# Optimization experiments

Measured on AMD Instinct MI355X. Metric: run time of the kernel, lower is better.

## Reference

```python
import jax, jax.numpy as jnp
import numpy as np
from jax import lax

SR = 7
HEADS = 8
EPS = 1e-5

def dwconv(x, w):
    # x: [B,C,H,W], w: [C,1,3,3] depthwise
    return lax.conv_general_dilated(x, w, (1, 1), 'SAME',
                                    feature_group_count=x.shape[1],
                                    dimension_numbers=('NCHW', 'OIHW', 'NCHW'))

def bn(x, g, b, m, v):
    # eval-mode BatchNorm2d over channel dim of [B,C,H,W]
    scale = g / jnp.sqrt(v + EPS)
    return x * scale[:, None, None] + (b - m * scale)[:, None, None]

def avgpool(x, k):
    B, C, H, W = x.shape
    return x.reshape(B, C, H // k, k, W // k, k).mean(axis=(3, 5))

def upsample(x, k):
    B, C, H, W = x.shape
    return jax.image.resize(x, (B, C, H * k, W * k), method='bilinear')


def setup_inputs() -> dict:
    key = jax.random.key(0)
    ks = jax.random.split(key, 12)
    B, N, C = 16, 3136, 256
    d = {}
    d['x'] = jax.random.normal(ks[0], (B, N, C), jnp.float32)
    d['Wv'] = jax.random.normal(ks[1], (C, C), jnp.float32) * 0.05
    d['conv1_w'] = jax.random.normal(ks[2], (C, 1, 3, 3), jnp.float32) * 0.05
    d['bn1_g'] = jnp.ones((C,), jnp.float32)
    d['bn1_b'] = jnp.zeros((C,), jnp.float32)
    d['bn1_m'] = jax.random.normal(ks[3], (C,), jnp.float32) * 0.05
    d['bn1_v'] = jax.random.uniform(ks[4], (C,), jnp.float32, 0.5, 1.5)
    d['conv2_w'] = jax.random.normal(ks[5], (C, 1, 3, 3), jnp.float32) * 0.05
    d['bn2_g'] = jnp.ones((C,), jnp.float32)
    d['bn2_b'] = jnp.zeros((C,), jnp.float32)
    d['bn2_m'] = jax.random.normal(ks[6], (C,), jnp.float32) * 0.05
    d['bn2_v'] = jax.random.uniform(ks[7], (C,), jnp.float32, 0.5, 1.5)
    d['vup_w'] = jax.random.normal(ks[8], (C, 1, 3, 3), jnp.float32) * 0.05
    d['bn3_g'] = jnp.ones((C,), jnp.float32)
    d['bn3_b'] = jnp.zeros((C,), jnp.float32)
    d['bn3_m'] = jax.random.normal(ks[9], (C,), jnp.float32) * 0.05
    d['bn3_v'] = jax.random.uniform(ks[10], (C,), jnp.float32, 0.5, 1.5)
    d['Wp'] = jax.random.normal(ks[11], (C, C), jnp.float32) * 0.05
    d['bp'] = jnp.zeros((C,), jnp.float32)
    return d


def reference(x, Wv, conv1_w, bn1_g, bn1_b, bn1_m, bn1_v,
              conv2_w, bn2_g, bn2_b, bn2_m, bn2_v,
              vup_w, bn3_g, bn3_b, bn3_m, bn3_v, Wp, bp):
    B, N, C = x.shape
    h = w = int(np.sqrt(N))
    hd = C // HEADS
    scale = C ** (-0.5)

    v = x @ Wv.T                                    # [B,N,C] (torch Linear, no bias)
    skip = v.reshape(B, h, w, C).transpose(0, 3, 1, 2)  # [B,C,h,w]

    s1 = bn(dwconv(skip, conv1_w), bn1_g, bn1_b, bn1_m, bn1_v)
    q = avgpool(s1, SR)                             # [B,C,h_,w_]
    s2 = bn(dwconv(jax.nn.gelu(s1, approximate=False), conv2_w),
            bn2_g, bn2_b, bn2_m, bn2_v)
    k = avgpool(s2, SR)                             # [B,C,h_,w_]
    skip_tok = jax.nn.gelu(s2, approximate=False).reshape(B, C, N).transpose(0, 2, 1)

    h_, w_ = h // SR, w // SR
    N_ = h_ * w_
    qh = q.reshape(B, HEADS, hd, N_).transpose(0, 1, 3, 2)   # [B,H,N_,d]
    kh = k.reshape(B, HEADS, hd, N_).transpose(0, 1, 3, 2)   # [B,H,N_,d]
    vh = v.reshape(B, N, HEADS, hd).transpose(0, 2, 1, 3)    # [B,H,N,d]

    attn = jnp.einsum('bhnd,bhmd->bhnm', qh, kh)             # [B,H,N_,N_]
    attn = attn.reshape(B * HEADS, N_, h_, w_)
    attn = upsample(attn, SR) * scale                        # [B*H,N_,h,w]
    attn = attn.reshape(B, HEADS, N_, N)
    attn = jax.nn.softmax(attn, axis=-1)

    o = jnp.einsum('bhnm,bhmd->bhnd', attn, vh)              # [B,H,N_,d]
    o = o.reshape(B, HEADS, h_, w_, hd).transpose(0, 1, 4, 2, 3).reshape(B, C, h_, w_)
    o = bn(dwconv(upsample(o, SR), vup_w), bn3_g, bn3_b, bn3_m, bn3_v)  # [B,C,h,w]

    out = o.reshape(B, C, N).transpose(0, 2, 1) + skip_tok
    out = out @ Wp.T + bp
    return out
```

## Files before the change

### kernel.cpp

```cpp
#include <hip/hip_runtime.h>
#include <math.h>

#define B_     16
#define H_IMG  56
#define W_IMG  56
#define N_TOK  3136
#define C_     256
#define C4_    64
#define NHEAD  8
#define HDIM   32
#define NCH    8

typedef float f32x4 __attribute__((ext_vector_type(4)));
typedef __bf16 bf16x8 __attribute__((ext_vector_type(8)));

__device__ __forceinline__ float geluf(float x) {
    return 0.5f * x * (1.0f + erff(x * 0.70710678118654752f));
}

__device__ __forceinline__ void up_coef(int o, int& i0, int& i1, float& t) {
    float f  = (float)(o - 3) * (1.0f / 7.0f);
    float fl = floorf(f);
    int   ii = (int)fl;
    t = f - fl;
    if (ii < 0)       { i0 = 0; i1 = 0; t = 0.0f; }
    else if (ii >= 7) { i0 = 7; i1 = 7; t = 0.0f; }
    else              { i0 = ii; i1 = ii + 1; }
}

__device__ __forceinline__ void split_bf16(float4 f, uint2& hi, uint2& lo) {
    unsigned u0 = __float_as_uint(f.x), u1 = __float_as_uint(f.y);
    unsigned u2 = __float_as_uint(f.z), u3 = __float_as_uint(f.w);
    unsigned h0 = u0 & 0xFFFF0000u, h1 = u1 & 0xFFFF0000u;
    unsigned h2 = u2 & 0xFFFF0000u, h3 = u3 & 0xFFFF0000u;
    hi = make_uint2((h0 >> 16) | h1, (h2 >> 16) | h3);
    float l0 = f.x - __uint_as_float(h0);
    float l1 = f.y - __uint_as_float(h1);
    float l2 = f.z - __uint_as_float(h2);
    float l3 = f.w - __uint_as_float(h3);
    lo = make_uint2((__float_as_uint(l0) >> 16) | (__float_as_uint(l1) & 0xFFFF0000u),
                    (__float_as_uint(l2) >> 16) | (__float_as_uint(l3) & 0xFFFF0000u));
}

__device__ __forceinline__ unsigned pack2_bf16(float a, float b) {
    __bf16 ha = (__bf16)a, hb = (__bf16)b;
    unsigned short ua = __builtin_bit_cast(unsigned short, ha);
    unsigned short ub = __builtin_bit_cast(unsigned short, hb);
    return (unsigned)ua | ((unsigned)ub << 16);
}

__global__ void prep_kernel(
    const float* __restrict__ w1, const float* __restrict__ w2, const float* __restrict__ w3,
    const float* __restrict__ g1, const float* __restrict__ b1, const float* __restrict__ m1, const float* __restrict__ v1,
    const float* __restrict__ g2, const float* __restrict__ b2, const float* __restrict__ m2, const float* __restrict__ v2,
    const float* __restrict__ g3, const float* __restrict__ b3, const float* __restrict__ m3, const float* __restrict__ v3,
    float* __restrict__ wT1, float* __restrict__ wT2, float* __restrict__ wT3,
    float* __restrict__ sc1, float* __restrict__ sh1,
    float* __restrict__ sc2, float* __restrict__ sh2,
    float* __restrict__ sc3, float* __restrict__ sh3)
{
    int c = threadIdx.x;
#pragma unroll
    for (int t = 0; t < 9; ++t) {
        wT1[t * C_ + c] = w1[c * 9 + t];
        wT2[t * C_ + c] = w2[c * 9 + t];
        wT3[t * C_ + c] = w3[c * 9 + t];
    }
    float s1 = g1[c] * rsqrtf(v1[c] + 1e-5f); sc1[c] = s1; sh1[c] = b1[c] - m1[c] * s1;
    float s2 = g2[c] * rsqrtf(v2[c] + 1e-5f); sc2[c] = s2; sh2[c] = b2[c] - m2[c] * s2;
    float s3 = g3[c] * rsqrtf(v3[c] + 1e-5f); sc3[c] = s3; sh3[c] = b3[c] - m3[c] * s3;
}

#define AHI 0
#define ALO 2560
#define BHI 5120
#define BLO 7680
__global__ __launch_bounds__(256, 2) void gemm_nt_mfma_kernel(
    const float* __restrict__ A,
    const float* __restrict__ Bm,
    const float* __restrict__ bias,
    float* __restrict__ C,
    int M, int N)
{
    __shared__ unsigned lds[10240];
    const int tid  = threadIdx.x;
    const int nb   = N >> 7;
    const int bx   = blockIdx.x % nb;
    const int by   = blockIdx.x / nb;
    const int lane = tid & 63;
    const int wv   = tid >> 6;
    const int wr   = wv >> 1, wc = wv & 1;
    const int l15  = lane & 15, kb = lane >> 4;

    const int srow = tid >> 1;
    const int sdw  = (tid & 1) * 8;
    const float* Ap = A  + (size_t)(by * 128 + srow) * 256 + (tid & 1) * 16;
    const float* Bp = Bm + (size_t)(bx * 128 + srow) * 256 + (tid & 1) * 16;

    f32x4 acc[4][4];
#pragma unroll
    for (int m = 0; m < 4; ++m)
#pragma unroll
        for (int n = 0; n < 4; ++n) acc[m][n] = (f32x4)(0.0f);

    float4 aP[2][4], bP[2][4];
#pragma unroll
    for (int i = 0; i < 4; ++i) {
        aP[0][i] = *(const float4*)(Ap + i * 4);
        bP[0][i] = *(const float4*)(Bp + i * 4);
    }
#pragma unroll
    for (int i = 0; i < 4; ++i) {
        aP[1][i] = *(const float4*)(Ap + 32 + i * 4);
        bP[1][i] = *(const float4*)(Bp + 32 + i * 4);
    }

#pragma unroll
    for (int k0 = 0; k0 < 256; k0 += 32) {
        const int sel = (k0 >> 5) & 1;
        __syncthreads();
        {
            uint2 h[4], l[4];
#pragma unroll
            for (int i = 0; i < 4; ++i) split_bf16(aP[sel][i], h[i], l[i]);
            *(uint4*)&lds[AHI + srow * 20 + sdw]     = make_uint4(h[0].x, h[0].y, h[1].x, h[1].y);
            *(uint4*)&lds[AHI + srow * 20 + sdw + 4] = make_uint4(h[2].x, h[2].y, h[3].x, h[3].y);
            *(uint4*)&lds[ALO + srow * 20 + sdw]     = make_uint4(l[0].x, l[0].y, l[1].x, l[1].y);
            *(uint4*)&lds[ALO + srow * 20 + sdw + 4] = make_uint4(l[2].x, l[2].y, l[3].x, l[3].y);
#pragma unroll
            for (int i = 0; i < 4; ++i) split_bf16(bP[sel][i], h[i], l[i]);
            *(uint4*)&lds[BHI + srow * 20 + sdw]     = make_uint4(h[0].x, h[0].y, h[1].x, h[1].y);
            *(uint4*)&lds[BHI + srow * 20 + sdw + 4] = make_uint4(h[2].x, h[2].y, h[3].x, h[3].y);
            *(uint4*)&lds[BLO + srow * 20 + sdw]     = make_uint4(l[0].x, l[0].y, l[1].x, l[1].y);
            *(uint4*)&lds[BLO + srow * 20 + sdw + 4] = make_uint4(l[2].x, l[2].y, l[3].x, l[3].y);
        }
        if (k0 + 64 < 256) {
#pragma unroll
            for (int i = 0; i < 4; ++i) aP[sel][i] = *(const float4*)(Ap + k0 + 64 + i * 4);
#pragma unroll
            for (int i = 0; i < 4; ++i) bP[sel][i] = *(const float4*)(Bp + k0 + 64 + i * 4);
        }
        __syncthreads();

        bf16x8 ah[4], al[4], bh[4], bl[4];
#pragma unroll
        for (int m = 0; m < 4; ++m) {
            int r = wr * 64 + m * 16 + l15;
            ah[m] = *(const bf16x8*)&lds[AHI + r * 20 + kb * 4];
            al[m] = *(const bf16x8*)&lds[ALO + r * 20 + kb * 4];
        }
#pragma unroll
        for (int n = 0; n < 4; ++n) {
            int r = wc * 64 + n * 16 + l15;
            bh[n] = *(const bf16x8*)&lds[BHI + r * 20 + kb * 4];
            bl[n] = *(const bf16x8*)&lds[BLO + r * 20 + kb * 4];
        }
#pragma unroll
        for (int m = 0; m < 4; ++m)
#pragma unroll
            for (int n = 0; n < 4; ++n) {
                acc[m][n] = __builtin_amdgcn_mfma_f32_16x16x32_bf16(ah[m], bh[n], acc[m][n], 0, 0, 0);
                acc[m][n] = __builtin_amdgcn_mfma_f32_16x16x32_bf16(ah[m], bl[n], acc[m][n], 0, 0, 0);
                acc[m][n] = __builtin_amdgcn_mfma_f32_16x16x32_bf16(al[m], bh[n], acc[m][n], 0, 0, 0);
            }
    }

    const int rb = by * 128 + wr * 64 + kb * 4;
    const int cb = bx * 128 + wc * 64 + l15;
#pragma unroll
    for (int n = 0; n < 4; ++n) {
        int col = cb + n * 16;
        float bv = bias ? bias[col] : 0.0f;
#pragma unroll
        for (int m = 0; m < 4; ++m) {
            int row = rb + m * 16;
#pragma unroll
            for (int r = 0; r < 4; ++r)
                C[(size_t)(row + r) * N + col] = acc[m][n][r] + bv;
        }
    }
}

__global__ __launch_bounds__(256, 4) void dwconv_bn_pool_gelu_kernel(
    const float* __restrict__ in, const float* __restrict__ wT,
    const float* __restrict__ scv, const float* __restrict__ shv,
    float* __restrict__ outg, float* __restrict__ pool)
{
    const int blk = blockIdx.x;
    const int xcd = blk & 7;
    const int j   = blk >> 3;
    const int b   = xcd + 8 * (j >> 6);
    const int g   = j & 63;
    const int gy  = g >> 3, gx = g & 7;
    const int tid = threadIdx.x;
    const int c4  = tid & 63;
    const int wv  = tid >> 6;
    const int c0  = c4 * 4;

    float4 wr[9];
#pragma unroll
    for (int t = 0; t < 9; ++t) wr[t] = *(const float4*)(wT + t * C_ + c0);
    const float4 sc = *(const float4*)(scv + c0);
    const float4 sh = *(const float4*)(shv + c0);

    const int x0 = gx * 7, y0 = gy * 7;
    const float* inb = in + (size_t)b * N_TOK * C_;
    float4 acc = make_float4(0, 0, 0, 0);

    for (int p = wv; p < 49; p += 4) {
        int py = p / 7, px = p - py * 7;
        int y = y0 + py, x = x0 + px;
        float cx = 0.f, cy = 0.f, cz = 0.f, cw = 0.f;
#pragma unroll
        for (int dy = -1; dy <= 1; ++dy) {
            int yy = y + dy;
            if (yy < 0 || yy >= H_IMG) continue;
#pragma unroll
            for (int dx = -1; dx <= 1; ++dx) {
                int xx = x + dx;
                if (xx < 0 || xx >= W_IMG) continue;
                const float4 iv = *(const float4*)(inb + (size_t)(yy * W_IMG + xx) * C_ + c0);
                const float4 w  = wr[(dy + 1) * 3 + (dx + 1)];
                cx = fmaf(iv.x, w.x, cx);
                cy = fmaf(iv.y, w.y, cy);
                cz = fmaf(iv.z, w.z, cz);
                cw = fmaf(iv.w, w.w, cw);
            }
        }
        float vx = cx * sc.x + sh.x;
        float vy = cy * sc.y + sh.y;
        float vz = cz * sc.z + sh.z;
        float vw = cw * sc.w + sh.w;
        acc.x += vx; acc.y += vy; acc.z += vz; acc.w += vw;
        *(float4*)(outg + ((size_t)b * N_TOK + y * W_IMG + x) * C_ + c0) =
            make_float4(geluf(vx), geluf(vy), geluf(vz), geluf(vw));
    }

    __shared__ float4 ps[4][64];
    ps[wv][c4] = acc;
    __syncthreads();
    if (tid < 64) {
        float4 s  = ps[0][tid];
        float4 t1 = ps[1][tid];
        float4 t2 = ps[2][tid];
        float4 t3 = ps[3][tid];
        const float r = 1.0f / 49.0f;
        *(float4*)(pool + ((size_t)b * 64 + g) * C_ + tid * 4) = make_float4(
            (s.x + t1.x + t2.x + t3.x) * r, (s.y + t1.y + t2.y + t3.y) * r,
            (s.z + t1.z + t2.z + t3.z) * r, (s.w + t1.w + t2.w + t3.w) * r);
    }
}

__global__ __launch_bounds__(256, 3) void dwconv_up_bn_add_kernel(
    const float* __restrict__ osm,
    const float* __restrict__ wT,
    const float* __restrict__ scv, const float* __restrict__ shv,
    const float* __restrict__ add_,
    float* __restrict__ out)
{
    const int blk = blockIdx.x;
    const int xcd = blk & 7;
    const int j   = blk >> 3;
    const int b   = xcd + 8 * (j >> 6);
    const int g   = j & 63;
    const int gy  = g >> 3, gx = g & 7;
    const int tid = threadIdx.x;
    const int c4  = tid & 63;
    const int wv  = tid >> 6;
    const int c0  = c4 * 4;

    float4 wr[9];
#pragma unroll
    for (int t = 0; t < 9; ++t) wr[t] = *(const float4*)(wT + t * C_ + c0);
    const float4 sc = *(const float4*)(scv + c0);
    const float4 sh = *(const float4*)(shv + c0);

    const float* ob = osm + (size_t)b * 64 * C_ + c0;
    const int cry0 = max(gy - 1, 0), cry1 = gy, cry2 = min(gy + 1, 7);
    const int crx0 = max(gx - 1, 0), crx1 = gx, crx2 = min(gx + 1, 7);

    for (int cpass = 0; cpass < 2; ++cpass) {
        const int xi = wv + cpass * 4;
        if (xi >= 7) break;
        const int x = gx * 7 + xi;

        float xt[3]; int rixv[3]; bool xval[3];
#pragma unroll
        for (int e = 0; e < 3; ++e) {
            int xx = x - 1 + e;
            xval[e] = (xx >= 0 && xx < W_IMG);
            if (xval[e]) {
                int i0, i1; float t;
                up_coef(xx, i0, i1, t);
                rixv[e] = i0 - gx + 1;
                xt[e]   = t;
            } else { rixv[e] = 0; xt[e] = 0.f; }
        }

        float4 CX[3][3];
#pragma unroll
        for (int ri = 0; ri < 3; ++ri) {
            const int rowc = (ri == 0) ? cry0 : ((ri == 1) ? cry1 : cry2);
            const float4 p0 = *(const float4*)(ob + (size_t)(rowc * 8 + crx0) * C_);
            const float4 p1 = *(const float4*)(ob + (size_t)(rowc * 8 + crx1) * C_);
            const float4 p2 = *(const float4*)(ob + (size_t)(rowc * 8 + crx2) * C_);
#pragma unroll
            for (int e = 0; e < 3; ++e) {
                const bool h2 = rixv[e] != 0;
                float lox = h2 ? p1.x : p0.x, hix = h2 ? p2.x : p1.x;
                float loy = h2 ? p1.y : p0.y, hiy = h2 ? p2.y : p1.y;
                float loz = h2 ? p1.z : p0.z, hiz = h2 ? p2.z : p1.z;
                float low = h2 ? p1.w : p0.w, hiw = h2 ? p2.w : p1.w;
                const float t = xt[e];
                float vx = fmaf(t, hix - lox, lox);
                float vy = fmaf(t, hiy - loy, loy);
                float vz = fmaf(t, hiz - loz, loz);
                float vw = fmaf(t, hiw - low, low);
                if (!xval[e]) { vx = vy = vz = vw = 0.f; }
                CX[ri][e] = make_float4(vx, vy, vz, vw);
            }
        }

#define UPROW(YY, U)                                                          \
        {                                                                     \
            int i0_, i1_; float t_;                                           \
            up_coef((YY), i0_, i1_, t_);                                      \
            const bool h2_ = (i0_ - gy + 1) != 0;                             \
            _Pragma("unroll")                                                 \
            for (int e = 0; e < 3; ++e) {                                     \
                const float4 lo = h2_ ? CX[1][e] : CX[0][e];                  \
                const float4 hi = h2_ ? CX[2][e] : CX[1][e];                  \
                U[e] = make_float4(fmaf(t_, hi.x - lo.x, lo.x),               \
                                   fmaf(t_, hi.y - lo.y, lo.y),               \
                                   fmaf(t_, hi.z - lo.z, lo.z),               \
                                   fmaf(t_, hi.w - lo.w, lo.w));              \
            }                                                                 \
        }

        float4 Um[3], U0[3], Up[3];
        UPROW(gy * 7 - 1, Um);
        UPROW(gy * 7,     U0);
#pragma unroll
        for (int y7 = 0; y7 < 7; ++y7) {
            const int y = gy * 7 + y7;
            UPROW(y + 1, Up);
            float ax = 0.f, ay = 0.f, az = 0.f, aw = 0.f;
            if (!(gy == 0 && y7 == 0)) {
#pragma unroll
                for (int e = 0; e < 3; ++e) {
                    const float4 w = wr[e];
                    ax = fmaf(Um[e].x, w.x, ax); ay = fmaf(Um[e].y, w.y, ay);
                    az = fmaf(Um[e].z, w.z, az); aw = fmaf(Um[e].w, w.w, aw);
                }
            }
#pragma unroll
            for (int e = 0; e < 3; ++e) {
                const float4 w = wr[3 + e];
                ax = fmaf(U0[e].x, w.x, ax); ay = fmaf(U0[e].y, w.y, ay);
                az = fmaf(U0[e].z, w.z, az); aw = fmaf(U0[e].w, w.w, aw);
            }
            if (!(gy == 7 && y7 == 6)) {
#pragma unroll
                for (int e = 0; e < 3; ++e) {
                    const float4 w = wr[6 + e];
                    ax = fmaf(Up[e].x, w.x, ax); ay = fmaf(Up[e].y, w.y, ay);
                    az = fmaf(Up[e].z, w.z, az); aw = fmaf(Up[e].w, w.w, aw);
                }
            }
            const size_t pix = (size_t)b * N_TOK + (size_t)y * W_IMG + x;
            const float4 av = *(const float4*)(add_ + pix * C_ + c0);
            *(float4*)(out + pix * C_ + c0) = make_float4(
                ax * sc.x + sh.x + av.x, ay * sc.y + sh.y + av.y,
                az * sc.z + sh.z + av.z, aw * sc.w + sh.w + av.w);
#pragma unroll
            for (int e = 0; e < 3; ++e) { Um[e] = U0[e]; U0[e] = Up[e]; }
        }
#undef UPROW
    }
}

__global__ __launch_bounds__(256) void qk_kernel(
    const float* __restrict__ q, const float* __restrict__ k,
    float* __restrict__ attnL, float* __restrict__ mrow_g)
{
    int bh = blockIdx.x;
    int b = bh >> 3, head = bh & 7;
    __shared__ float qs[64][33];
    __shared__ float ks[64][33];
    int tid = threadIdx.x;
    for (int t = tid; t < 512; t += 256) {
        int i = t >> 3, dq = (t & 7) * 4;
        const float4 qv = *(const float4*)(q + ((size_t)(b * 64 + i) * C_ + head * 32 + dq));
        const float4 kv = *(const float4*)(k + ((size_t)(b * 64 + i) * C_ + head * 32 + dq));
        qs[i][dq + 0] = qv.x; qs[i][dq + 1] = qv.y; qs[i][dq + 2] = qv.z; qs[i][dq + 3] = qv.w;
        ks[i][dq + 0] = kv.x; ks[i][dq + 1] = kv.y; ks[i][dq + 2] = kv.z; ks[i][dq + 3] = kv.w;
    }
    __syncthreads();
    int i  = tid >> 2;
    int jb = (tid & 3) * 16;
    float qr[32];
#pragma unroll
    for (int d = 0; d < 32; ++d) qr[d] = qs[i][d];
    float* outp = attnL + (size_t)bh * 4096 + i * 64 + jb;
    float mloc = -1e30f;
#pragma unroll
    for (int j = 0; j < 16; ++j) {
        float s = 0.f;
#pragma unroll
        for (int d = 0; d < 32; ++d) s = fmaf(qr[d], ks[jb + j][d], s);
        float sv = s * 0.0625f;
        outp[j] = sv;
        mloc = fmaxf(mloc, sv);
    }
    mloc = fmaxf(mloc, __shfl_xor(mloc, 1));
    mloc = fmaxf(mloc, __shfl_xor(mloc, 2));
    if ((tid & 3) == 0) mrow_g[bh * 64 + i] = mloc;
}

#define S_ALS 0
#define S_P   1792
#define S_VH  4096
#define S_VL  5248
#define S_RY  6400
#define S_ZP  7168
__global__ __launch_bounds__(256, 4) void attn_pv_kernel(
    const float* __restrict__ attnL,
    const float* __restrict__ mrow_g,
    const float* __restrict__ v,
    float* __restrict__ part_o,
    float* __restrict__ part_z)
{
    __shared__ unsigned sm[7424];
    float* smf = (float*)sm;

    const int blk   = blockIdx.x;
    const int xcd   = blk & 7;
    const int r8    = blk >> 3;
    const int b     = xcd + 8 * (r8 >> 6);
    const int rem   = r8 & 63;
    const int head  = rem >> 3;
    const int chunk = rem & 7;
    const int bh    = b * 8 + head;
    const int jb    = min(max(chunk - 1, 0), 5);

    const int tid  = threadIdx.x;
    const int lane = tid & 63;
    const int w    = tid >> 6;
    const int l15  = lane & 15, kb = lane >> 4;
    const int i    = tid >> 2;
    const int dg   = tid & 3;

    for (int u = tid; u < 384; u += 256) {
        int row = u / 6, cc = u % 6;
        float4 va = *(const float4*)(attnL + (size_t)bh * 4096 + row * 64 + jb * 8 + cc * 4);
        *(float4*)&smf[S_ALS + row * 28 + cc * 4] = va;
    }
    sm[S_P + (tid >> 2) * 36 + 28 + (tid & 3)] = 0;
    {
        int base = (tid < 128) ? S_VH : S_VL;
        int q2 = tid & 127;
        sm[base + (q2 >> 2) * 36 + 28 + (q2 & 3)] = 0;
    }
    const float mr = mrow_g[bh * 64 + i];

    int   x0a[14]; float txa[14];
#pragma unroll
    for (int j = 0; j < 14; ++j) {
        int i0, i1; float t;
        up_coef(dg * 14 + j, i0, i1, t);
        x0a[j] = i0; txa[j] = t;
    }

    f32x4 acc[2];
    acc[0] = (f32x4)(0.0f); acc[1] = (f32x4)(0.0f);
    float zacc = 0.0f;

    for (int rr = 0; rr < 7; ++rr) {
        const int y = chunk * 7 + rr;
        __syncthreads();

        float4 va, vb;
        if (tid < 224) {
            int x2 = tid >> 3, d0 = (tid & 7) * 4;
            const float* vp = v + ((size_t)b * N_TOK + y * W_IMG + 2 * x2) * C_ + head * 32 + d0;
            va = *(const float4*)vp;
            vb = *(const float4*)(vp + C_);
        }
        {
            int y0, y1; float ty;
            up_coef(y, y0, y1, ty);
#pragma unroll
            for (int kk2 = dg; kk2 < 9; kk2 += 4) {
                int ks2 = kk2 < 8 ? kk2 : 7;
                float a0 = smf[S_ALS + i * 28 + (y0 - jb) * 8 + ks2];
                float a1 = smf[S_ALS + i * 28 + (y1 - jb) * 8 + ks2];
                smf[S_RY + i * 12 + kk2] = fmaf(ty, a1 - a0, a0) - mr;
            }
        }
        if (tid < 224) {
            int x2 = tid >> 3, d0 = (tid & 7) * 4;
            float ae[4] = {va.x, va.y, va.z, va.w};
            float be[4] = {vb.x, vb.y, vb.z, vb.w};
#pragma unroll
            for (int j = 0; j < 4; ++j) {
                unsigned ua = __float_as_uint(ae[j]), ha = ua & 0xFFFF0000u;
                unsigned ub = __float_as_uint(be[j]), hb2 = ub & 0xFFFF0000u;
                sm[S_VH + (d0 + j) * 36 + x2] = (ha >> 16) | hb2;
                float la = ae[j] - __uint_as_float(ha);
                float lb = be[j] - __uint_as_float(hb2);
                sm[S_VL + (d0 + j) * 36 + x2] =
                    (__float_as_uint(la) >> 16) | (__float_as_uint(lb) & 0xFFFF0000u);
            }
        }
        __syncthreads();

#pragma unroll
        for (int j = 0; j < 7; ++j) {
            float r0 = smf[S_RY + i * 12 + x0a[2 * j]];
            float r1 = smf[S_RY + i * 12 + x0a[2 * j] + 1];
            float l0 = fmaf(txa[2 * j], r1 - r0, r0);
            float r2 = smf[S_RY + i * 12 + x0a[2 * j + 1]];
            float r3 = smf[S_RY + i * 12 + x0a[2 * j + 1] + 1];
            float l1 = fmaf(txa[2 * j + 1], r3 - r2, r2);
            float p0 = __expf(l0), p1 = __expf(l1);
            zacc += p0 + p1;
            sm[S_P + i * 36 + dg * 7 + j] = pack2_bf16(p0, p1);
        }
        __syncthreads();

#pragma unroll
        for (int s = 0; s < 2; ++s) {
            bf16x8 pa = *(const bf16x8*)&sm[S_P + (w * 16 + l15) * 36 + s * 16 + kb * 4];
#pragma unroll
            for (int n = 0; n < 2; ++n) {
                bf16x8 bhv = *(const bf16x8*)&sm[S_VH + (n * 16 + l15) * 36 + s * 16 + kb * 4];
                bf16x8 blv = *(const bf16x8*)&sm[S_VL + (n * 16 + l15) * 36 + s * 16 + kb * 4];
                acc[n] = __builtin_amdgcn_mfma_f32_16x16x32_bf16(pa, bhv, acc[n], 0, 0, 0);
                acc[n] = __builtin_amdgcn_mfma_f32_16x16x32_bf16(pa, blv, acc[n], 0, 0, 0);
            }
        }
    }

    smf[S_ZP + i * 4 + dg] = zacc;
    __syncthreads();
    if (tid < 64) {
        float zt = smf[S_ZP + tid * 4] + smf[S_ZP + tid * 4 + 1] +
                   smf[S_ZP + tid * 4 + 2] + smf[S_ZP + tid * 4 + 3];
        part_z[((size_t)bh * NCH + chunk) * 64 + tid] = zt;
    }
    const int row4 = (lane >> 4) * 4;
#pragma unroll
    for (int n = 0; n < 2; ++n)
#pragma unroll
        for (int r2 = 0; r2 < 4; ++r2) {
            int i2 = w * 16 + row4 + r2;
            int d  = n * 16 + l15;
            part_o[(((size_t)bh * NCH + chunk) * 64 + i2) * 32 + d] = acc[n][r2];
        }
}

__global__ __launch_bounds__(256) void combine_kernel(
    const float* __restrict__ part_o, const float* __restrict__ part_z,
    float* __restrict__ o_small)
{
    int idx = blockIdx.x * 256 + threadIdx.x;
    if (idx >= B_ * 64 * C_) return;
    int c = idx % C_;
    int g = (idx / C_) % 64;
    int b = idx / (C_ * 64);
    int head = c >> 5, d = c & 31;
    int bh = b * 8 + head;
    float oo = 0.f, zz = 0.f;
    for (int ch = 0; ch < NCH; ++ch) {
        oo += part_o[(((size_t)bh * NCH + ch) * 64 + g) * 32 + d];
        zz += part_z[((size_t)bh * NCH + ch) * 64 + g];
    }
    o_small[idx] = oo / zz;
}

extern "C" void kernel_launch(void* const* d_in, const int* in_sizes, int n_in,
                              void* d_out, int out_size, void* d_ws, size_t ws_size,
                              hipStream_t stream)
{
    const float* x    = (const float*)d_in[0];
    const float* Wv   = (const float*)d_in[1];
    const float* c1w  = (const float*)d_in[2];
    const float* b1g  = (const float*)d_in[3];
    const float* b1b  = (const float*)d_in[4];
    const float* b1m  = (const float*)d_in[5];
    const float* b1v  = (const float*)d_in[6];
    const float* c2w  = (const float*)d_in[7];
    const float* b2g  = (const float*)d_in[8];
    const float* b2b  = (const float*)d_in[9];
    const float* b2m  = (const float*)d_in[10];
    const float* b2v  = (const float*)d_in[11];
    const float* vupw = (const float*)d_in[12];
    const float* b3g  = (const float*)d_in[13];
    const float* b3b  = (const float*)d_in[14];
    const float* b3m  = (const float*)d_in[15];
    const float* b3v  = (const float*)d_in[16];
    const float* Wp   = (const float*)d_in[17];
    const float* bp   = (const float*)d_in[18];
    float* out = (float*)d_out;
    float* ws  = (float*)d_ws;

    const size_t SZ = (size_t)B_ * N_TOK * C_;
    float* v       = ws;
    float* s1g     = v   + SZ;
    float* s2g     = s1g + SZ;
    float* q       = s2g + SZ;
    float* kk      = q  + (size_t)B_ * 64 * C_;
    float* attnL   = kk + (size_t)B_ * 64 * C_;
    float* part_o  = attnL  + (size_t)B_ * 8 * 64 * 64;
    float* part_z  = part_o + (size_t)B_ * 8 * NCH * 64 * 32;
    float* o_small = part_z + (size_t)B_ * 8 * NCH * 64;
    float* wT1     = o_small + (size_t)B_ * 64 * C_;
    float* wT2     = wT1 + 9 * C_;
    float* wT3     = wT2 + 9 * C_;
    float* sc1     = wT3 + 9 * C_;
    float* sh1     = sc1 + C_;
    float* sc2     = sh1 + C_;
    float* sh2     = sc2 + C_;
    float* sc3     = sh2 + C_;
    float* sh3     = sc3 + C_;
    float* mrow_g  = sh3 + C_;

    const int M = B_ * N_TOK;

    prep_kernel<<<1, 256, 0, stream>>>(c1w, c2w, vupw,
        b1g, b1b, b1m, b1v, b2g, b2b, b2m, b2v, b3g, b3b, b3m, b3v,
        wT1, wT2, wT3, sc1, sh1, sc2, sh2, sc3, sh3);
    gemm_nt_mfma_kernel<<<(M / 128) * (C_ / 128), 256, 0, stream>>>(x, Wv, nullptr, v, M, C_);
    dwconv_bn_pool_gelu_kernel<<<1024, 256, 0, stream>>>(v, wT1, sc1, sh1, s1g, q);
    dwconv_bn_pool_gelu_kernel<<<1024, 256, 0, stream>>>(s1g, wT2, sc2, sh2, s2g, kk);
    qk_kernel<<<B_ * 8, 256, 0, stream>>>(q, kk, attnL, mrow_g);
    attn_pv_kernel<<<B_ * 8 * NCH, 256, 0, stream>>>(attnL, mrow_g, v, part_o, part_z);
    combine_kernel<<<B_ * 64 * C_ / 256, 256, 0, stream>>>(part_o, part_z, o_small);
    dwconv_up_bn_add_kernel<<<1024, 256, 0, stream>>>(o_small, wT3, sc3, sh3, s2g, v);
    gemm_nt_mfma_kernel<<<(M / 128) * (C_ / 128), 256, 0, stream>>>(v, Wp, bp, out, M, C_);
}
```

Before: 212.1 us.

## Pre-split GEMM weights to bf16 hi/lo and load operands directly without LDS

Adds a small kernel that splits each weight matrix into bf16 high and low halves once per call. The GEMM now drops its shared-memory staging and barriers, reading A straight from global memory in MFMA fragment layout (splitting it in registers) and reading the pre-split B halves directly. This removes the LDS traffic, the syncthreads and the per-block re-splitting of weights. In exchange, global loads are strided and no longer coalesced, there is no software prefetch, and A is re-read by both column blocks, relying on cache.

```diff
diff --git a/kernel.cpp b/kernel.cpp
--- a/kernel.cpp
+++ b/kernel.cpp
@@ -71,18 +71,26 @@
     float s3 = g3[c] * rsqrtf(v3[c] + 1e-5f); sc3[c] = s3; sh3[c] = b3[c] - m3[c] * s3;
 }
 
-#define AHI 0
-#define ALO 2560
-#define BHI 5120
-#define BLO 7680
+__global__ __launch_bounds__(256) void split_w_kernel(
+    const float* __restrict__ W, unsigned short* __restrict__ Bh,
+    unsigned short* __restrict__ Bl)
+{
+    int idx = blockIdx.x * 256 + threadIdx.x;
+    float4 f = ((const float4*)W)[idx];
+    uint2 h, l;
+    split_bf16(f, h, l);
+    ((uint2*)Bh)[idx] = h;
+    ((uint2*)Bl)[idx] = l;
+}
+
 __global__ __launch_bounds__(256, 2) void gemm_nt_mfma_kernel(
     const float* __restrict__ A,
-    const float* __restrict__ Bm,
+    const unsigned short* __restrict__ Bh,
+    const unsigned short* __restrict__ Bl,
     const float* __restrict__ bias,
     float* __restrict__ C,
     int M, int N)
 {
-    __shared__ unsigned lds[10240];
     const int tid  = threadIdx.x;
     const int nb   = N >> 7;
     const int bx   = blockIdx.x % nb;
@@ -92,10 +100,9 @@
     const int wr   = wv >> 1, wc = wv & 1;
     const int l15  = lane & 15, kb = lane >> 4;
 
-    const int srow = tid >> 1;
-    const int sdw  = (tid & 1) * 8;
-    const float* Ap = A  + (size_t)(by * 128 + srow) * 256 + (tid & 1) * 16;
-    const float* Bp = Bm + (size_t)(bx * 128 + srow) * 256 + (tid & 1) * 16;
+    const float* Ab = A + (size_t)(by * 128 + wr * 64 + l15) * 256 + kb * 8;
+    const unsigned short* Bhb = Bh + (size_t)(bx * 128 + wc * 64 + l15) * 256 + kb * 8;
+    const unsigned short* Blb = Bl + (size_t)(bx * 128 + wc * 64 + l15) * 256 + kb * 8;
 
     f32x4 acc[4][4];
 #pragma unroll
@@ -103,57 +110,24 @@
 #pragma unroll
         for (int n = 0; n < 4; ++n) acc[m][n] = (f32x4)(0.0f);
 
-    float4 aP[2][4], bP[2][4];
-#pragma unroll
-    for (int i = 0; i < 4; ++i) {
-        aP[0][i] = *(const float4*)(Ap + i * 4);
-        bP[0][i] = *(const float4*)(Bp + i * 4);
-    }
-#pragma unroll
-    for (int i = 0; i < 4; ++i) {
-        aP[1][i] = *(const float4*)(Ap + 32 + i * 4);
-        bP[1][i] = *(const float4*)(Bp + 32 + i * 4);
-    }
-
 #pragma unroll
     for (int k0 = 0; k0 < 256; k0 += 32) {
-        const int sel = (k0 >> 5) & 1;
-        __syncthreads();
-        {
-            uint2 h[4], l[4];
-#pragma unroll
-            for (int i = 0; i < 4; ++i) split_bf16(aP[sel][i], h[i], l[i]);
-            *(uint4*)&lds[AHI + srow * 20 + sdw]     = make_uint4(h[0].x, h[0].y, h[1].x, h[1].y);
-            *(uint4*)&lds[AHI + srow * 20 + sdw + 4] = make_uint4(h[2].x, h[2].y, h[3].x, h[3].y);
-            *(uint4*)&lds[ALO + srow * 20 + sdw]     = make_uint4(l[0].x, l[0].y, l[1].x, l[1].y);
-            *(uint4*)&lds[ALO + srow * 20 + sdw + 4] = make_uint4(l[2].x, l[2].y, l[3].x, l[3].y);
-#pragma unroll
-            for (int i = 0; i < 4; ++i) split_bf16(bP[sel][i], h[i], l[i]);
-            *(uint4*)&lds[BHI + srow * 20 + sdw]     = make_uint4(h[0].x, h[0].y, h[1].x, h[1].y);
-            *(uint4*)&lds[BHI + srow * 20 + sdw + 4] = make_uint4(h[2].x, h[2].y, h[3].x, h[3].y);
-            *(uint4*)&lds[BLO + srow * 20 + sdw]     = make_uint4(l[0].x, l[0].y, l[1].x, l[1].y);
-            *(uint4*)&lds[BLO + srow * 20 + sdw + 4] = make_uint4(l[2].x, l[2].y, l[3].x, l[3].y);
-        }
-        if (k0 + 64 < 256) {
-#pragma unroll
-            for (int i = 0; i < 4; ++i) aP[sel][i] = *(const float4*)(Ap + k0 + 64 + i * 4);
-#pragma unroll
-            for (int i = 0; i < 4; ++i) bP[sel][i] = *(const float4*)(Bp + k0 + 64 + i * 4);
-        }
-        __syncthreads();
-
         bf16x8 ah[4], al[4], bh[4], bl[4];
 #pragma unroll
+        for (int n = 0; n < 4; ++n) {
+            bh[n] = *(const bf16x8*)(Bhb + (size_t)(n * 16) * 256 + k0);
+            bl[n] = *(const bf16x8*)(Blb + (size_t)(n * 16) * 256 + k0);
+        }
+#pragma unroll
         for (int m = 0; m < 4; ++m) {
-            int r = wr * 64 + m * 16 + l15;
-            ah[m] = *(const bf16x8*)&lds[AHI + r * 20 + kb * 4];
-            al[m] = *(const bf16x8*)&lds[ALO + r * 20 + kb * 4];
-        }
-#pragma unroll
-        for (int n = 0; n < 4; ++n) {
-            int r = wc * 64 + n * 16 + l15;
-            bh[n] = *(const bf16x8*)&lds[BHI + r * 20 + kb * 4];
-            bl[n] = *(const bf16x8*)&lds[BLO + r * 20 + kb * 4];
+            const float* ap = Ab + (size_t)(m * 16) * 256 + k0;
+            float4 f0 = *(const float4*)ap;
+            float4 f1 = *(const float4*)(ap + 4);
+            uint2 h0, l0, h1, l1;
+            split_bf16(f0, h0, l0);
+            split_bf16(f1, h1, l1);
+            ah[m] = __builtin_bit_cast(bf16x8, make_uint4(h0.x, h0.y, h1.x, h1.y));
+            al[m] = __builtin_bit_cast(bf16x8, make_uint4(l0.x, l0.y, l1.x, l1.y));
         }
 #pragma unroll
         for (int m = 0; m < 4; ++m)
@@ -624,18 +598,24 @@
     float* sc3     = sh2 + C_;
     float* sh3     = sc3 + C_;
     float* mrow_g  = sh3 + C_;
+    unsigned short* WvH = (unsigned short*)(mrow_g + B_ * 8 * 64);
+    unsigned short* WvL = WvH + 65536;
+    unsigned short* WpH = WvL + 65536;
+    unsigned short* WpL = WpH + 65536;
 
     const int M = B_ * N_TOK;
 
     prep_kernel<<<1, 256, 0, stream>>>(c1w, c2w, vupw,
         b1g, b1b, b1m, b1v, b2g, b2b, b2m, b2v, b3g, b3b, b3m, b3v,
         wT1, wT2, wT3, sc1, sh1, sc2, sh2, sc3, sh3);
-    gemm_nt_mfma_kernel<<<(M / 128) * (C_ / 128), 256, 0, stream>>>(x, Wv, nullptr, v, M, C_);
+    split_w_kernel<<<64, 256, 0, stream>>>(Wv, WvH, WvL);
+    split_w_kernel<<<64, 256, 0, stream>>>(Wp, WpH, WpL);
+    gemm_nt_mfma_kernel<<<(M / 128) * (C_ / 128), 256, 0, stream>>>(x, WvH, WvL, nullptr, v, M, C_);
     dwconv_bn_pool_gelu_kernel<<<1024, 256, 0, stream>>>(v, wT1, sc1, sh1, s1g, q);
     dwconv_bn_pool_gelu_kernel<<<1024, 256, 0, stream>>>(s1g, wT2, sc2, sh2, s2g, kk);
     qk_kernel<<<B_ * 8, 256, 0, stream>>>(q, kk, attnL, mrow_g);
     attn_pv_kernel<<<B_ * 8 * NCH, 256, 0, stream>>>(attnL, mrow_g, v, part_o, part_z);
     combine_kernel<<<B_ * 64 * C_ / 256, 256, 0, stream>>>(part_o, part_z, o_small);
     dwconv_up_bn_add_kernel<<<1024, 256, 0, stream>>>(o_small, wT3, sc3, sh3, s2g, v);
-    gemm_nt_mfma_kernel<<<(M / 128) * (C_ / 128), 256, 0, stream>>>(v, Wp, bp, out, M, C_);
-}
+    gemm_nt_mfma_kernel<<<(M / 128) * (C_ / 128), 256, 0, stream>>>(v, WpH, WpL, bp, out, M, C_);
+}
```

After: 276.2 us. 30.3% more time.

## Load GEMM tiles directly into LDS with swizzle, split to bf16 after LDS read

Applied to the files above, without the earlier changes.

The GEMM mainloop now uses global_load_lds to copy fp32 A/B tiles straight into shared memory, with an XOR swizzle to avoid bank conflicts. The bf16 hi/lo split moves from the store side to after the LDS read. This removes the register prefetch buffers and the VGPR round trip on the load path. In exchange, the split work is repeated per wave, there is no double-buffered prefetch so loads are exposed behind the barrier, and LDS traffic in fp32 is larger.

```diff
diff --git a/kernel.cpp b/kernel.cpp
--- a/kernel.cpp
+++ b/kernel.cpp
@@ -49,6 +49,12 @@
     return (unsigned)ua | ((unsigned)ub << 16);
 }
 
+__device__ __forceinline__ void gload_lds16(const float* g, float* l) {
+    __builtin_amdgcn_global_load_lds(
+        (const __attribute__((address_space(1))) unsigned int*)g,
+        (__attribute__((address_space(3))) unsigned int*)l, 16, 0, 0);
+}
+
 __global__ void prep_kernel(
     const float* __restrict__ w1, const float* __restrict__ w2, const float* __restrict__ w3,
     const float* __restrict__ g1, const float* __restrict__ b1, const float* __restrict__ m1, const float* __restrict__ v1,
@@ -71,10 +77,6 @@
     float s3 = g3[c] * rsqrtf(v3[c] + 1e-5f); sc3[c] = s3; sh3[c] = b3[c] - m3[c] * s3;
 }
 
-#define AHI 0
-#define ALO 2560
-#define BHI 5120
-#define BLO 7680
 __global__ __launch_bounds__(256, 2) void gemm_nt_mfma_kernel(
     const float* __restrict__ A,
     const float* __restrict__ Bm,
@@ -82,7 +84,7 @@
     float* __restrict__ C,
     int M, int N)
 {
-    __shared__ unsigned lds[10240];
+    __shared__ float lds[8192];
     const int tid  = threadIdx.x;
     const int nb   = N >> 7;
     const int bx   = blockIdx.x % nb;
@@ -92,10 +94,8 @@
     const int wr   = wv >> 1, wc = wv & 1;
     const int l15  = lane & 15, kb = lane >> 4;
 
-    const int srow = tid >> 1;
-    const int sdw  = (tid & 1) * 8;
-    const float* Ap = A  + (size_t)(by * 128 + srow) * 256 + (tid & 1) * 16;
-    const float* Bp = Bm + (size_t)(bx * 128 + srow) * 256 + (tid & 1) * 16;
+    const float* Abase = A  + (size_t)(by * 128) * 256;
+    const float* Bbase = Bm + (size_t)(bx * 128) * 256;
 
     f32x4 acc[4][4];
 #pragma unroll
@@ -103,42 +103,26 @@
 #pragma unroll
         for (int n = 0; n < 4; ++n) acc[m][n] = (f32x4)(0.0f);
 
-    float4 aP[2][4], bP[2][4];
+    int srow[4], ssk[4];
 #pragma unroll
     for (int i = 0; i < 4; ++i) {
-        aP[0][i] = *(const float4*)(Ap + i * 4);
-        bP[0][i] = *(const float4*)(Bp + i * 4);
-    }
-#pragma unroll
-    for (int i = 0; i < 4; ++i) {
-        aP[1][i] = *(const float4*)(Ap + 32 + i * 4);
-        bP[1][i] = *(const float4*)(Bp + 32 + i * 4);
+        int u = i * 256 + tid;
+        srow[i] = u >> 3;
+        ssk[i]  = ((u & 7) ^ (srow[i] & 7)) << 2;
     }
 
 #pragma unroll
     for (int k0 = 0; k0 < 256; k0 += 32) {
-        const int sel = (k0 >> 5) & 1;
         __syncthreads();
-        {
-            uint2 h[4], l[4];
-#pragma unroll
-            for (int i = 0; i < 4; ++i) split_bf16(aP[sel][i], h[i], l[i]);
-            *(uint4*)&lds[AHI + srow * 20 + sdw]     = make_uint4(h[0].x, h[0].y, h[1].x, h[1].y);
-            *(uint4*)&lds[AHI + srow * 20 + sdw + 4] = make_uint4(h[2].x, h[2].y, h[3].x, h[3].y);
-            *(uint4*)&lds[ALO + srow * 20 + sdw]     = make_uint4(l[0].x, l[0].y, l[1].x, l[1].y);
-            *(uint4*)&lds[ALO + srow * 20 + sdw + 4] = make_uint4(l[2].x, l[2].y, l[3].x, l[3].y);
-#pragma unroll
-            for (int i = 0; i < 4; ++i) split_bf16(bP[sel][i], h[i], l[i]);
-            *(uint4*)&lds[BHI + srow * 20 + sdw]     = make_uint4(h[0].x, h[0].y, h[1].x, h[1].y);
-            *(uint4*)&lds[BHI + srow * 20 + sdw + 4] = make_uint4(h[2].x, h[2].y, h[3].x, h[3].y);
-            *(uint4*)&lds[BLO + srow * 20 + sdw]     = make_uint4(l[0].x, l[0].y, l[1].x, l[1].y);
-            *(uint4*)&lds[BLO + srow * 20 + sdw + 4] = make_uint4(l[2].x, l[2].y, l[3].x, l[3].y);
-        }
-        if (k0 + 64 < 256) {
-#pragma unroll
-            for (int i = 0; i < 4; ++i) aP[sel][i] = *(const float4*)(Ap + k0 + 64 + i * 4);
-#pragma unroll
-            for (int i = 0; i < 4; ++i) bP[sel][i] = *(const float4*)(Bp + k0 + 64 + i * 4);
+#pragma unroll
+        for (int i = 0; i < 4; ++i) {
+            int u = i * 256 + tid;
+            gload_lds16(Abase + (size_t)srow[i] * 256 + k0 + ssk[i], &lds[u * 4]);
+        }
+#pragma unroll
+        for (int i = 0; i < 4; ++i) {
+            int u = i * 256 + tid;
+            gload_lds16(Bbase + (size_t)srow[i] * 256 + k0 + ssk[i], &lds[4096 + u * 4]);
         }
         __syncthreads();
 
@@ -146,14 +130,24 @@
 #pragma unroll
         for (int m = 0; m < 4; ++m) {
             int r = wr * 64 + m * 16 + l15;
-            ah[m] = *(const bf16x8*)&lds[AHI + r * 20 + kb * 4];
-            al[m] = *(const bf16x8*)&lds[ALO + r * 20 + kb * 4];
+            float4 f0 = *(const float4*)&lds[r * 32 + ((((kb * 2)    ) ^ (r & 7)) << 2)];
+            float4 f1 = *(const float4*)&lds[r * 32 + ((((kb * 2) + 1) ^ (r & 7)) << 2)];
+            uint2 h0, l0, h1, l1;
+            split_bf16(f0, h0, l0);
+            split_bf16(f1, h1, l1);
+            ah[m] = __builtin_bit_cast(bf16x8, make_uint4(h0.x, h0.y, h1.x, h1.y));
+            al[m] = __builtin_bit_cast(bf16x8, make_uint4(l0.x, l0.y, l1.x, l1.y));
         }
 #pragma unroll
         for (int n = 0; n < 4; ++n) {
             int r = wc * 64 + n * 16 + l15;
-            bh[n] = *(const bf16x8*)&lds[BHI + r * 20 + kb * 4];
-            bl[n] = *(const bf16x8*)&lds[BLO + r * 20 + kb * 4];
+            float4 f0 = *(const float4*)&lds[4096 + r * 32 + ((((kb * 2)    ) ^ (r & 7)) << 2)];
+            float4 f1 = *(const float4*)&lds[4096 + r * 32 + ((((kb * 2) + 1) ^ (r & 7)) << 2)];
+            uint2 h0, l0, h1, l1;
+            split_bf16(f0, h0, l0);
+            split_bf16(f1, h1, l1);
+            bh[n] = __builtin_bit_cast(bf16x8, make_uint4(h0.x, h0.y, h1.x, h1.y));
+            bl[n] = __builtin_bit_cast(bf16x8, make_uint4(l0.x, l0.y, l1.x, l1.y));
         }
 #pragma unroll
         for (int m = 0; m < 4; ++m)
```

New measurement: 217.2 us. 2.4% more time.
